# Kernel tuning notes

Hardware: AMD Instinct MI355X
Metric: run time of the kernel (lower is better)

The kernel has to match this reference:

```python
import jax, jax.numpy as jnp
import numpy as np

N = 50000
DIN, DH, DOUT = 128, 128, 64
DEPTH = 3
TEMP = 1.0
WEIGHT = 0.5
LN_EPS = 1e-5
E_RAND = 1_600_000


def setup_inputs() -> dict:
    key = jax.random.key(0)
    ks = jax.random.split(key, 16)
    x = jax.random.normal(ks[0], (N, DIN), jnp.float32)
    # random edges + ring (guarantees degree >= 2 after symmetrization)
    src = jax.random.randint(ks[1], (E_RAND,), 0, N)
    dst = jax.random.randint(ks[2], (E_RAND,), 0, N)
    ring = jnp.arange(N)
    s = jnp.concatenate([src, ring])
    d = jnp.concatenate([dst, (ring + 1) % N])
    edge_index = jnp.stack([jnp.concatenate([s, d]), jnp.concatenate([d, s])]).astype(jnp.int64)  # [2, 3.3M], symmetric

    def glorot(k, i, o):
        return jax.random.normal(k, (i, o), jnp.float32) * jnp.sqrt(2.0 / (i + o)).astype(jnp.float32)

    return {
        "x": x, "edge_index": edge_index,
        "W0": glorot(ks[3], DIN, DH), "b0": jnp.zeros((DH,), jnp.float32),
        "W1": glorot(ks[4], DH, DH),  "b1": jnp.zeros((DH,), jnp.float32),
        "W2": glorot(ks[5], DH, DH),  "b2": jnp.zeros((DH,), jnp.float32),
        "W_out": glorot(ks[6], DH, DOUT), "b_out": jnp.zeros((DOUT,), jnp.float32),
        "gamma": jnp.ones((DH,), jnp.float32), "beta": jnp.zeros((DH,), jnp.float32),
    }


def _seg(vals, idx):
    return jax.ops.segment_sum(vals, idx, num_segments=N)


def _gcn_conv(h_in, W, b, src, dst):
    # PyG GCNConv: self-loops, sym norm D^-1/2 (A+I) D^-1/2
    h = h_in @ W
    ones = jnp.ones(src.shape, jnp.float32)
    deg = _seg(ones, dst) + 1.0  # degree incl. self-loop
    dinv = jax.lax.rsqrt(deg)
    msg = h[src] * (dinv[src] * dinv[dst])[:, None]
    return _seg(msg, dst) + h * (1.0 / deg)[:, None] + b


def _layernorm(x, g, b):
    m = jnp.mean(x, axis=-1, keepdims=True)
    v = jnp.mean((x - m) ** 2, axis=-1, keepdims=True)
    return (x - m) * jax.lax.rsqrt(v + LN_EPS) * g + b


def reference(x, edge_index, W0, b0, W1, b1, W2, b2, W_out, b_out, gamma, beta):
    src, dst = edge_index[0], edge_index[1]
    h = x
    for W, b in ((W0, b0), (W1, b1), (W2, b2)):
        h = _layernorm(jax.nn.relu(_gcn_conv(h, W, b, src, dst)), gamma, beta)
    emb = _gcn_conv(h, W_out, b_out, src, dst)  # [N, DOUT]

    # --- entropy gradient (edge-list form of the dense-A einsums) ---
    ones = jnp.ones(src.shape, jnp.float32)
    deg_adj = _seg(ones, src)                     # row sums of A (no self-loops)
    en_norm = 1.0 / jnp.sqrt(deg_adj * DH)        # uses hidden_dim, as in the original

    rn2 = jnp.sum(emb * emb, axis=1)              # ||X_i||^2
    dot = jnp.sum(emb[src] * emb[dst], axis=1)    # <X_i, X_j> per edge
    res1 = deg_adj * rn2
    res2 = _seg(dot, src)
    res3 = _seg(rn2[dst], src)
    energies = 0.5 * (res1 - 2.0 * res2 + res3) * en_norm  # normalize_energies=True

    logits = -energies / TEMP
    P = jax.nn.softmax(logits, axis=0) + 1e-10
    logP = jnp.log(P)
    S = -jnp.sum(P * logP)
    Pbar = P * (S + logP)                         # [N]

    nsumX = _seg(emb[dst], src)                   # sum_j A_ij X_j
    nsumP = _seg(Pbar[dst], src)                  # sum_j A_ij Pbar_j
    XP = emb * Pbar[:, None]
    g1 = deg_adj[:, None] * XP
    g2 = emb * nsumP[:, None]
    g3 = Pbar[:, None] * nsumX
    g4 = _seg(XP[dst], src)
    grad_S = (g1 + g2 - g3 - g4) / TEMP * en_norm[:, None]

    return emb + WEIGHT * grad_S
```

## Files before the change

kernel.cpp:

```cpp
#include <hip/hip_runtime.h>
#include <hip/hip_fp16.h>

#define DIN 128
#define DH  128
#define DFO 64
#define LN_EPS 1e-5f
#define WEIGHT 0.5f

#define MAXB  104
#define CAPB  48
#define FLUSH 32
#define SENT  0xFFFFFFFFu

typedef unsigned int uint32;
typedef unsigned short ushort16;

__device__ __forceinline__ float h_lo(uint32 u) { return __half2float(__ushort_as_half((unsigned short)(u & 0xFFFFu))); }
__device__ __forceinline__ float h_hi(uint32 u) { return __half2float(__ushort_as_half((unsigned short)(u >> 16))); }
__device__ __forceinline__ uint32 pack_h2(float a, float b) {
  return (uint32)__half_as_ushort(__float2half_rn(a)) | ((uint32)__half_as_ushort(__float2half_rn(b)) << 16);
}
__device__ __forceinline__ int sb(uint32 u, int k) { return ((int)(u << (24 - 8 * k))) >> 24; }

__device__ __forceinline__ float wave_sum(float v) {
  #pragma unroll
  for (int off = 32; off > 0; off >>= 1) v += __shfl_xor(v, off);
  return v;
}
__device__ __forceinline__ float wave_max(float v) {
  #pragma unroll
  for (int off = 32; off > 0; off >>= 1) v = fmaxf(v, __shfl_xor(v, off));
  return v;
}

__device__ __forceinline__ void fq16(float* a, uint4 u, float w) {
  #pragma unroll
  for (int k = 0; k < 4; ++k) a[k]      = fmaf((float)sb(u.x, k), w, a[k]);
  #pragma unroll
  for (int k = 0; k < 4; ++k) a[4 + k]  = fmaf((float)sb(u.y, k), w, a[4 + k]);
  #pragma unroll
  for (int k = 0; k < 4; ++k) a[8 + k]  = fmaf((float)sb(u.z, k), w, a[8 + k]);
  #pragma unroll
  for (int k = 0; k < 4; ++k) a[12 + k] = fmaf((float)sb(u.w, k), w, a[12 + k]);
}

__global__ __launch_bounds__(64) void k_prep(const float* __restrict__ g, const float* __restrict__ b,
                      const float* __restrict__ W1, const float* __restrict__ W2,
                      const float* __restrict__ Wo, float* __restrict__ Wg1,
                      float* __restrict__ Wg2, float* __restrict__ Wgo,
                      float* __restrict__ vecs) {
  int c = blockIdx.x * 64 + threadIdx.x;
  const float* W; float* Wg; float* gv; float* bv; int ld; int col;
  if (c < 128)      { W = W1; Wg = Wg1; gv = vecs;       bv = vecs + 128; ld = 128; col = c; }
  else if (c < 256) { W = W2; Wg = Wg2; gv = vecs + 256; bv = vecs + 384; ld = 128; col = c - 128; }
  else              { W = Wo; Wg = Wgo; gv = vecs + 512; bv = vecs + 576; ld = 64;  col = c - 256; }
  float gs = 0.f, bs = 0.f;
  for (int k = 0; k < 128; ++k) {
    float w = W[k * ld + col];
    float gk = g[k];
    Wg[k * ld + col] = gk * w;
    gs += gk * w;
    bs += b[k] * w;
  }
  gv[col] = gs; bv[col] = bs;
}

__global__ __launch_bounds__(256) void k_bin3(const int* __restrict__ src, const int* __restrict__ dst,
                       int E2, int nbc, int GCAP, int* __restrict__ gbcnt,
                       uint32* __restrict__ gpairs) {
  __shared__ uint32 lbuf[MAXB][CAPB];
  __shared__ int lcnt[MAXB];
  __shared__ int fbase[MAXB];
  __shared__ int fm[MAXB];
  __shared__ short flist[MAXB];
  __shared__ int fn;
  int wv = threadIdx.x >> 6, ln = threadIdx.x & 63;
  for (int b = threadIdx.x; b < nbc; b += 256) lcnt[b] = 0;
  __syncthreads();

  for (int base = blockIdx.x * 256; base < E2; base += gridDim.x * 256) {
    int i = base + threadIdx.x;
    if (i < E2) {
      int s = src[i], d = dst[i];
      int b0 = s >> 9;
      uint32 v0 = ((uint32)(s & 511) << 16) | (uint32)d;
      int sl = atomicAdd(&lcnt[b0], 1);
      if (sl < CAPB) lbuf[b0][sl] = v0;
      else { int g = atomicAdd(&gbcnt[b0 * 16], 1); gpairs[(size_t)b0 * GCAP + g] = v0; }
      int b1 = d >> 9;
      uint32 v1 = ((uint32)(d & 511) << 16) | (uint32)s;
      sl = atomicAdd(&lcnt[b1], 1);
      if (sl < CAPB) lbuf[b1][sl] = v1;
      else { int g = atomicAdd(&gbcnt[b1 * 16], 1); gpairs[(size_t)b1 * GCAP + g] = v1; }
    }
    if (threadIdx.x == 0) fn = 0;
    __syncthreads();
    if (threadIdx.x < nbc) {
      int m = lcnt[threadIdx.x];
      if (m >= FLUSH) {
        if (m > CAPB) m = CAPB;
        int r = (m + 15) & ~15;
        fbase[threadIdx.x] = atomicAdd(&gbcnt[threadIdx.x * 16], r);
        fm[threadIdx.x] = m;
        int fi = atomicAdd(&fn, 1);
        flist[fi] = (short)threadIdx.x;
      }
    }
    __syncthreads();
    int nf = fn;
    for (int fi = wv; fi < nf; fi += 4) {
      int b = flist[fi];
      int m = fm[b], r = (m + 15) & ~15, g = fbase[b];
      if (ln < r)
        gpairs[(size_t)b * GCAP + g + ln] = (ln < m) ? lbuf[b][ln] : SENT;
    }
    __syncthreads();
    if (threadIdx.x < nbc && lcnt[threadIdx.x] >= FLUSH) lcnt[threadIdx.x] = 0;
    __syncthreads();
  }
  if (threadIdx.x < nbc) {
    int m = lcnt[threadIdx.x]; if (m > CAPB) m = CAPB;
    fm[threadIdx.x] = m;
    if (m > 0) {
      int r = (m + 15) & ~15;
      fbase[threadIdx.x] = atomicAdd(&gbcnt[threadIdx.x * 16], r);
    }
  }
  __syncthreads();
  for (int b = wv; b < nbc; b += 4) {
    int m = fm[b];
    if (m > 0) {
      int r = (m + 15) & ~15, g = fbase[b];
      if (ln < r)
        gpairs[(size_t)b * GCAP + g + ln] = (ln < m) ? lbuf[b][ln] : SENT;
    }
  }
}

__global__ __launch_bounds__(1024) void k_csr(const uint32* __restrict__ gpairs, const int* __restrict__ gbcnt,
                      int GCAP, int GCAPC, int N, int* __restrict__ rowbeg, int* __restrict__ rowcnt,
                      float* __restrict__ dinv, float* __restrict__ cntf, ushort16* __restrict__ col) {
  __shared__ int hist[512];
  __shared__ int pos[512];
  int b = blockIdx.x, tid = threadIdx.x;
  if (tid < 512) hist[tid] = 0;
  __syncthreads();
  int m = gbcnt[b * 16];
  const uint32* pp = gpairs + (size_t)b * GCAP;
  for (int t = tid; t < m; t += 1024) {
    uint32 v = pp[t];
    if (v != SENT) atomicAdd(&hist[v >> 16], 1);
  }
  __syncthreads();
  int cnt = (tid < 512) ? hist[tid] : 0;
  for (int off = 1; off < 512; off <<= 1) {
    int u = (tid >= off && tid < 512) ? hist[tid - off] : 0;
    __syncthreads();
    if (tid < 512) hist[tid] += u;
    __syncthreads();
  }
  int cbase = b * GCAPC;
  if (tid < 512) {
    int excl = hist[tid] - cnt;
    pos[tid] = excl;
    int node = (b << 9) + tid;
    if (node < N) {
      rowbeg[node] = cbase + excl;
      rowcnt[node] = cnt;
      cntf[node] = (float)cnt;
      dinv[node] = rsqrtf((float)cnt + 1.0f);
    }
  }
  __syncthreads();
  for (int t = tid; t < m; t += 1024) {
    uint32 v = pp[t];
    if (v != SENT) {
      int sl = atomicAdd(&pos[v >> 16], 1);
      col[cbase + sl] = (ushort16)(v & 0xFFFFu);
    }
  }
}

template <int COLS, int MODE>
__global__ __launch_bounds__(256) void k_gemm(const void* __restrict__ Ap, const float* __restrict__ W,
                            const float* __restrict__ dinv, const float2* __restrict__ stats,
                            const float* __restrict__ gW, const float* __restrict__ bW,
                            uint32* __restrict__ qout, float* __restrict__ qsc, int N) {
  const int CG  = COLS / 4;
  const int RG  = 256 / CG;
  const int RPT = 64 / RG;
  __shared__ float4 At4[64 * 32];
  int t = threadIdx.x;
  int rbase = blockIdx.x * 64;
  #pragma unroll
  for (int i2 = 0; i2 < 8; ++i2) {
    int idx = t + 256 * i2;
    int row = idx >> 5, c4i = idx & 31;
    int gr = rbase + row;
    float4 v = make_float4(0.f, 0.f, 0.f, 0.f);
    if (gr < N) {
      if (MODE == 1) {
        const uint2* A2 = (const uint2*)Ap;
        uint2 p = A2[(size_t)(c4i >> 4) * N * 16 + (size_t)gr * 16 + (c4i & 15)];
        v = make_float4(h_lo(p.x), h_hi(p.x), h_lo(p.y), h_hi(p.y));
      } else {
        v = ((const float4*)Ap)[(size_t)gr * 32 + c4i];
      }
    }
    At4[idx] = v;
  }
  __syncthreads();
  int c4 = t % CG, rg = t / CG;
  float acc[RPT][4];
  #pragma unroll
  for (int r = 0; r < RPT; ++r) { acc[r][0] = acc[r][1] = acc[r][2] = acc[r][3] = 0.f; }
  const float4* W4 = (const float4*)W;
  #pragma unroll 2
  for (int k4 = 0; k4 < 32; ++k4) {
    float4 w0 = W4[(k4 * 4 + 0) * CG + c4];
    float4 w1 = W4[(k4 * 4 + 1) * CG + c4];
    float4 w2 = W4[(k4 * 4 + 2) * CG + c4];
    float4 w3 = W4[(k4 * 4 + 3) * CG + c4];
    #pragma unroll
    for (int r = 0; r < RPT; ++r) {
      float4 av = At4[(rg * RPT + r) * 32 + k4];
      acc[r][0] = fmaf(av.x, w0.x, acc[r][0]); acc[r][0] = fmaf(av.y, w1.x, acc[r][0]);
      acc[r][0] = fmaf(av.z, w2.x, acc[r][0]); acc[r][0] = fmaf(av.w, w3.x, acc[r][0]);
      acc[r][1] = fmaf(av.x, w0.y, acc[r][1]); acc[r][1] = fmaf(av.y, w1.y, acc[r][1]);
      acc[r][1] = fmaf(av.z, w2.y, acc[r][1]); acc[r][1] = fmaf(av.w, w3.y, acc[r][1]);
      acc[r][2] = fmaf(av.x, w0.z, acc[r][2]); acc[r][2] = fmaf(av.y, w1.z, acc[r][2]);
      acc[r][2] = fmaf(av.z, w2.z, acc[r][2]); acc[r][2] = fmaf(av.w, w3.z, acc[r][2]);
      acc[r][3] = fmaf(av.x, w0.w, acc[r][3]); acc[r][3] = fmaf(av.y, w1.w, acc[r][3]);
      acc[r][3] = fmaf(av.z, w2.w, acc[r][3]); acc[r][3] = fmaf(av.w, w3.w, acc[r][3]);
    }
  }
  float4 g4 = make_float4(0.f, 0.f, 0.f, 0.f), b4 = make_float4(0.f, 0.f, 0.f, 0.f);
  if (MODE == 1) { g4 = ((const float4*)gW)[c4]; b4 = ((const float4*)bW)[c4]; }
  int pl = c4 >> 4, slot = c4 & 15;
  #pragma unroll
  for (int r = 0; r < RPT; ++r) {
    int gr = rbase + rg * RPT + r;
    float o0 = 0.f, o1 = 0.f, o2 = 0.f, o3 = 0.f;
    if (gr < N) {
      float s = dinv[gr];
      if (MODE == 1) {
        float2 st = stats[gr];
        o0 = s * (st.y * (acc[r][0] - st.x * g4.x) + b4.x);
        o1 = s * (st.y * (acc[r][1] - st.x * g4.y) + b4.y);
        o2 = s * (st.y * (acc[r][2] - st.x * g4.z) + b4.z);
        o3 = s * (st.y * (acc[r][3] - st.x * g4.w) + b4.w);
      } else {
        o0 = acc[r][0] * s; o1 = acc[r][1] * s; o2 = acc[r][2] * s; o3 = acc[r][3] * s;
      }
    }
    float mx = fmaxf(fmaxf(fabsf(o0), fabsf(o1)), fmaxf(fabsf(o2), fabsf(o3)));
    #pragma unroll
    for (int m = 1; m < CG; m <<= 1) mx = fmaxf(mx, __shfl_xor(mx, m));
    if (gr < N) {
      float inv = (mx > 0.f) ? 127.f / mx : 0.f;
      int q0 = (int)rintf(o0 * inv), q1 = (int)rintf(o1 * inv);
      int q2 = (int)rintf(o2 * inv), q3 = (int)rintf(o3 * inv);
      uint32 qw = (uint32)(q0 & 255) | ((uint32)(q1 & 255) << 8) |
                  ((uint32)(q2 & 255) << 16) | ((uint32)(q3 & 255) << 24);
      qout[(size_t)pl * N * 16 + (size_t)gr * 16 + slot] = qw;
      if (c4 == 0) qsc[gr] = mx * (1.f / 127.f);
    }
  }
}

template <int PLANE>
__global__ __launch_bounds__(64) void k_aggh(const uint4* __restrict__ hq4, const float* __restrict__ hsc,
                      const int* __restrict__ rowbeg, const int* __restrict__ rowcnt,
                      const ushort16* __restrict__ col, const float* __restrict__ dinv,
                      const float* __restrict__ bias, uint4* __restrict__ vh4,
                      float2* __restrict__ ss, float2* __restrict__ stats, int N) {
  int i = blockIdx.x, lane = threadIdx.x;
  int f4 = lane & 3, sl = lane >> 2;
  const uint4* hp = hq4 + (size_t)PLANE * N * 4;
  int beg = rowbeg[i], end = beg + rowcnt[i];
  float a[16];
  #pragma unroll
  for (int k = 0; k < 16; ++k) a[k] = 0.f;
  if (lane < 4) fq16(a, hp[(size_t)i * 4 + f4], hsc[i]);
  int t = beg + sl;
  for (; t + 16 < end; t += 32) {
    int j0 = col[t], j1 = col[t + 16];
    float s0 = hsc[j0], s1 = hsc[j1];
    uint4 u0 = hp[(size_t)j0 * 4 + f4];
    uint4 u1 = hp[(size_t)j1 * 4 + f4];
    fq16(a, u0, s0); fq16(a, u1, s1);
  }
  if (t < end) { int j = col[t]; fq16(a, hp[(size_t)j * 4 + f4], hsc[j]); }
  #pragma unroll
  for (int k = 0; k < 16; ++k) {
    a[k] += __shfl_xor(a[k], 4);  a[k] += __shfl_xor(a[k], 8);
    a[k] += __shfl_xor(a[k], 16); a[k] += __shfl_xor(a[k], 32);
  }
  if (lane < 4) {
    float di = dinv[i];
    const float4* bb = (const float4*)bias + PLANE * 16 + f4 * 4;
    float s = 0.f, s2 = 0.f;
    #pragma unroll
    for (int q = 0; q < 4; ++q) {
      float4 b4 = bb[q];
      float v0 = fmaxf(fmaf(a[q*4+0], di, b4.x), 0.f);
      float v1 = fmaxf(fmaf(a[q*4+1], di, b4.y), 0.f);
      float v2 = fmaxf(fmaf(a[q*4+2], di, b4.z), 0.f);
      float v3 = fmaxf(fmaf(a[q*4+3], di, b4.w), 0.f);
      a[q*4+0] = v0; a[q*4+1] = v1; a[q*4+2] = v2; a[q*4+3] = v3;
      s += (v0 + v1) + (v2 + v3);
      s2 += (v0*v0 + v1*v1) + (v2*v2 + v3*v3);
    }
    s += __shfl_xor(s, 1); s2 += __shfl_xor(s2, 1);
    s += __shfl_xor(s, 2); s2 += __shfl_xor(s2, 2);
    uint4 o0, o1;
    o0.x = pack_h2(a[0], a[1]);  o0.y = pack_h2(a[2], a[3]);
    o0.z = pack_h2(a[4], a[5]);  o0.w = pack_h2(a[6], a[7]);
    o1.x = pack_h2(a[8], a[9]);  o1.y = pack_h2(a[10], a[11]);
    o1.z = pack_h2(a[12], a[13]); o1.w = pack_h2(a[14], a[15]);
    vh4[(size_t)PLANE * N * 8 + (size_t)i * 8 + f4 * 2]     = o0;
    vh4[(size_t)PLANE * N * 8 + (size_t)i * 8 + f4 * 2 + 1] = o1;
    if (lane == 0) {
      if (PLANE == 0) {
        ss[i] = make_float2(s, s2);
      } else {
        float2 qq = ss[i];
        float S = s + qq.x, S2 = s2 + qq.y;
        float mean = S * (1.f / 128.f);
        float var  = S2 * (1.f / 128.f) - mean * mean;
        stats[i] = make_float2(mean, rsqrtf(var + LN_EPS));
      }
    }
  }
}

__global__ __launch_bounds__(64) void k_agg_out(const uint4* __restrict__ hq4, const float* __restrict__ hsc,
                          const int* __restrict__ rowbeg, const int* __restrict__ rowcnt,
                          const ushort16* __restrict__ col, const float* __restrict__ dinv,
                          const float* __restrict__ bias, float* __restrict__ embf,
                          uint4* __restrict__ embq4, float* __restrict__ esc,
                          float* __restrict__ rn2, int N) {
  int i = blockIdx.x, lane = threadIdx.x;
  int f4 = lane & 3, sl = lane >> 2;
  int beg = rowbeg[i], end = beg + rowcnt[i];
  float a[16];
  #pragma unroll
  for (int k = 0; k < 16; ++k) a[k] = 0.f;
  if (lane < 4) fq16(a, hq4[(size_t)i * 4 + f4], hsc[i]);
  int t = beg + sl;
  for (; t + 16 < end; t += 32) {
    int j0 = col[t], j1 = col[t + 16];
    float s0 = hsc[j0], s1 = hsc[j1];
    uint4 u0 = hq4[(size_t)j0 * 4 + f4];
    uint4 u1 = hq4[(size_t)j1 * 4 + f4];
    fq16(a, u0, s0); fq16(a, u1, s1);
  }
  if (t < end) { int j = col[t]; fq16(a, hq4[(size_t)j * 4 + f4], hsc[j]); }
  #pragma unroll
  for (int k = 0; k < 16; ++k) {
    a[k] += __shfl_xor(a[k], 4);  a[k] += __shfl_xor(a[k], 8);
    a[k] += __shfl_xor(a[k], 16); a[k] += __shfl_xor(a[k], 32);
  }
  if (lane < 4) {
    float di = dinv[i];
    const float4* bb = (const float4*)bias + f4 * 4;
    float s2 = 0.f, mx = 0.f;
    #pragma unroll
    for (int q = 0; q < 4; ++q) {
      float4 b4 = bb[q];
      float e0 = fmaf(a[q*4+0], di, b4.x);
      float e1 = fmaf(a[q*4+1], di, b4.y);
      float e2 = fmaf(a[q*4+2], di, b4.z);
      float e3 = fmaf(a[q*4+3], di, b4.w);
      a[q*4+0] = e0; a[q*4+1] = e1; a[q*4+2] = e2; a[q*4+3] = e3;
      s2 += (e0*e0 + e1*e1) + (e2*e2 + e3*e3);
      mx = fmaxf(mx, fmaxf(fmaxf(fabsf(e0), fabsf(e1)), fmaxf(fabsf(e2), fabsf(e3))));
      ((float4*)embf)[(size_t)i * 16 + f4 * 4 + q] = make_float4(e0, e1, e2, e3);
    }
    s2 += __shfl_xor(s2, 1); s2 += __shfl_xor(s2, 2);
    mx = fmaxf(mx, __shfl_xor(mx, 1)); mx = fmaxf(mx, __shfl_xor(mx, 2));
    float inv = (mx > 0.f) ? 127.f / mx : 0.f;
    uint4 qo;
    uint32* qw = (uint32*)&qo;
    #pragma unroll
    for (int q = 0; q < 4; ++q) {
      int q0 = (int)rintf(a[q*4+0] * inv), q1 = (int)rintf(a[q*4+1] * inv);
      int q2 = (int)rintf(a[q*4+2] * inv), q3 = (int)rintf(a[q*4+3] * inv);
      qw[q] = (uint32)(q0 & 255) | ((uint32)(q1 & 255) << 8) |
              ((uint32)(q2 & 255) << 16) | ((uint32)(q3 & 255) << 24);
    }
    embq4[(size_t)i * 4 + f4] = qo;
    if (lane == 0) { rn2[i] = s2; esc[i] = mx * (1.f / 127.f); }
  }
}

__global__ __launch_bounds__(64) void k_passA(const float* __restrict__ embf, const uint4* __restrict__ embq4,
                        const float* __restrict__ esc, const int* __restrict__ rowbeg,
                        const int* __restrict__ rowcnt, const ushort16* __restrict__ col,
                        const float* __restrict__ rn2, const float* __restrict__ cntf,
                        float* __restrict__ nsumX, float* __restrict__ logits, int N) {
  int i = blockIdx.x, lane = threadIdx.x;
  int f4 = lane & 3, sl = lane >> 2;
  int beg = rowbeg[i], end = beg + rowcnt[i];
  float a[16];
  #pragma unroll
  for (int k = 0; k < 16; ++k) a[k] = 0.f;
  float r3 = 0.f;
  int t = beg + sl;
  for (; t + 16 < end; t += 32) {
    int j0 = col[t], j1 = col[t + 16];
    float s0 = esc[j0], s1 = esc[j1];
    uint4 u0 = embq4[(size_t)j0 * 4 + f4];
    uint4 u1 = embq4[(size_t)j1 * 4 + f4];
    fq16(a, u0, s0); fq16(a, u1, s1);
    if (f4 == 0) r3 += rn2[j0] + rn2[j1];
  }
  if (t < end) {
    int j = col[t];
    fq16(a, embq4[(size_t)j * 4 + f4], esc[j]);
    if (f4 == 0) r3 += rn2[j];
  }
  #pragma unroll
  for (int k = 0; k < 16; ++k) {
    a[k] += __shfl_xor(a[k], 4);  a[k] += __shfl_xor(a[k], 8);
    a[k] += __shfl_xor(a[k], 16); a[k] += __shfl_xor(a[k], 32);
  }
  r3 = wave_sum(r3);
  if (lane < 4) {
    float dd = 0.f;
    #pragma unroll
    for (int q = 0; q < 4; ++q) {
      float4 e = ((const float4*)embf)[(size_t)i * 16 + f4 * 4 + q];
      dd += e.x * a[q*4+0] + e.y * a[q*4+1] + e.z * a[q*4+2] + e.w * a[q*4+3];
      ((float4*)nsumX)[(size_t)i * 16 + f4 * 4 + q] = make_float4(a[q*4+0], a[q*4+1], a[q*4+2], a[q*4+3]);
    }
    dd += __shfl_xor(dd, 1); dd += __shfl_xor(dd, 2);
    if (lane == 0) {
      float c = cntf[i];
      float en = rsqrtf(c * 128.0f);
      logits[i] = -0.5f * (c * rn2[i] - 2.f * dd + r3) * en;
    }
  }
}

__global__ __launch_bounds__(256) void k_sm1(const float* __restrict__ logits, int N,
                                             float4* __restrict__ partials) {
  int idx = blockIdx.x * 256 + threadIdx.x;
  int w = threadIdx.x >> 6, ln = threadIdx.x & 63;
  float x = (idx < N) ? logits[idx] : -3.4e38f;
  float m = wave_max(x);
  __shared__ float red[3][4];
  if (ln == 0) red[0][w] = m;
  __syncthreads();
  float M = fmaxf(fmaxf(red[0][0], red[0][1]), fmaxf(red[0][2], red[0][3]));
  float ev = (idx < N) ? expf(x - M) : 0.f;
  float tv = (idx < N) ? (x - M) * ev : 0.f;
  float se = wave_sum(ev), st = wave_sum(tv);
  if (ln == 0) { red[1][w] = se; red[2][w] = st; }
  __syncthreads();
  if (threadIdx.x == 0)
    partials[blockIdx.x] = make_float4(M, red[1][0] + red[1][1] + red[1][2] + red[1][3],
                                          red[2][0] + red[2][1] + red[2][2] + red[2][3], 0.f);
}

__global__ __launch_bounds__(256) void k_sm2(const float4* __restrict__ partials, int nb,
                                             float* __restrict__ scal) {
  int tid = threadIdx.x;
  int w = tid >> 6, ln = tid & 63;
  float4 p = (tid < nb) ? partials[tid] : make_float4(-3.4e38f, 0.f, 0.f, 0.f);
  float m = wave_max(p.x);
  __shared__ float red[3][4];
  if (ln == 0) red[0][w] = m;
  __syncthreads();
  float M = fmaxf(fmaxf(red[0][0], red[0][1]), fmaxf(red[0][2], red[0][3]));
  float sc = (tid < nb) ? expf(p.x - M) : 0.f;
  float se = p.y * sc;
  float tt = (p.z + (p.x - M) * p.y) * sc;
  se = wave_sum(se); tt = wave_sum(tt);
  if (ln == 0) { red[1][w] = se; red[2][w] = tt; }
  __syncthreads();
  if (tid == 0) {
    float SE = red[1][0] + red[1][1] + red[1][2] + red[1][3];
    float TT = red[2][0] + red[2][1] + red[2][2] + red[2][3];
    scal[0] = M;
    scal[1] = SE;
    scal[2] = logf(SE) - TT / SE;
  }
}

__global__ __launch_bounds__(256) void k_pbar(const float* __restrict__ logits, int N,
                     const float* __restrict__ scal, float* __restrict__ Pb) {
  float M = scal[0], SE = scal[1], S = scal[2];
  int i = blockIdx.x * blockDim.x + threadIdx.x;
  int stride = gridDim.x * blockDim.x;
  for (; i < N; i += stride) {
    float p = expf(logits[i] - M) / SE + 1e-10f;
    Pb[i] = p * (S + logf(p));
  }
}

__global__ __launch_bounds__(64) void k_passB(const float* __restrict__ embf, const uint4* __restrict__ embq4,
                        const float* __restrict__ esc, const int* __restrict__ rowbeg,
                        const int* __restrict__ rowcnt, const ushort16* __restrict__ col,
                        const float* __restrict__ Pb, const float* __restrict__ cntf,
                        float* __restrict__ outp, int N) {
  int i = blockIdx.x, lane = threadIdx.x;
  int f4 = lane & 3, sl = lane >> 2;
  int beg = rowbeg[i], end = beg + rowcnt[i];
  float a[16];
  #pragma unroll
  for (int k = 0; k < 16; ++k) a[k] = 0.f;
  float sp = 0.f;
  int t = beg + sl;
  for (; t + 16 < end; t += 32) {
    int j0 = col[t], j1 = col[t + 16];
    float p0 = Pb[j0], p1 = Pb[j1];
    float w0 = p0 * esc[j0], w1 = p1 * esc[j1];
    uint4 u0 = embq4[(size_t)j0 * 4 + f4];
    uint4 u1 = embq4[(size_t)j1 * 4 + f4];
    fq16(a, u0, w0); fq16(a, u1, w1);
    if (f4 == 0) sp += p0 + p1;
  }
  if (t < end) {
    int j = col[t];
    float p = Pb[j];
    fq16(a, embq4[(size_t)j * 4 + f4], p * esc[j]);
    if (f4 == 0) sp += p;
  }
  #pragma unroll
  for (int k = 0; k < 16; ++k) {
    a[k] += __shfl_xor(a[k], 4);  a[k] += __shfl_xor(a[k], 8);
    a[k] += __shfl_xor(a[k], 16); a[k] += __shfl_xor(a[k], 32);
  }
  sp = wave_sum(sp);
  if (lane < 4) {
    float Pi = Pb[i];
    float c = cntf[i];
    float wgt = WEIGHT * rsqrtf(c * 128.0f);
    #pragma unroll
    for (int q = 0; q < 4; ++q) {
      float4 e = ((const float4*)embf)[(size_t)i * 16 + f4 * 4 + q];
      float4 n = ((const float4*)outp)[(size_t)i * 16 + f4 * 4 + q];
      float g0 = c * e.x * Pi + e.x * sp - Pi * n.x - a[q*4+0];
      float g1 = c * e.y * Pi + e.y * sp - Pi * n.y - a[q*4+1];
      float g2 = c * e.z * Pi + e.z * sp - Pi * n.z - a[q*4+2];
      float g3 = c * e.w * Pi + e.w * sp - Pi * n.w - a[q*4+3];
      ((float4*)outp)[(size_t)i * 16 + f4 * 4 + q] =
          make_float4(fmaf(wgt, g0, e.x), fmaf(wgt, g1, e.y), fmaf(wgt, g2, e.z), fmaf(wgt, g3, e.w));
    }
  }
}

extern "C" void kernel_launch(void* const* d_in, const int* in_sizes, int n_in,
                              void* d_out, int out_size, void* d_ws, size_t ws_size,
                              hipStream_t stream) {
  const float* x     = (const float*)d_in[0];
  const int*   ei    = (const int*)d_in[1];
  const float* W0    = (const float*)d_in[2];
  const float* b0    = (const float*)d_in[3];
  const float* W1    = (const float*)d_in[4];
  const float* b1    = (const float*)d_in[5];
  const float* W2    = (const float*)d_in[6];
  const float* b2    = (const float*)d_in[7];
  const float* Wo    = (const float*)d_in[8];
  const float* bo    = (const float*)d_in[9];
  const float* gamma = (const float*)d_in[10];
  const float* beta  = (const float*)d_in[11];

  int N = in_sizes[0] / DIN;
  int E = in_sizes[1] / 2;
  int E2 = E / 2;
  const int* src = ei;
  const int* dst = ei + E;
  int nbc = (N + 511) >> 9;
  int perb = E / nbc;
  int GCAP  = ((perb + perb / 3 + 8192) + 15) & ~15;
  int GCAPC = perb + 4096;

  char* w = (char*)d_ws;
  auto alloc = [&](size_t bytes) { void* p = w; w += (bytes + 255) & ~(size_t)255; return p; };
  char* regA = (char*)alloc((size_t)N * 128 * 2);
  char* regB = (char*)alloc((size_t)N * 64 * 2);
  char* pad  = (char*)alloc((size_t)2 * 1024 * 1024);
  (void)pad;
  ushort16* colx = (ushort16*)alloc((size_t)nbc * GCAPC * 2);
  int*    rowbeg = (int*)alloc((size_t)N * 4);
  int*    rowcnt = (int*)alloc((size_t)N * 4);
  float*  dinv   = (float*)alloc((size_t)N * 4);
  float*  cntf   = (float*)alloc((size_t)N * 4);
  float*  rn2    = (float*)alloc((size_t)N * 4);
  float*  logits = (float*)alloc((size_t)N * 4);
  float*  Pb     = (float*)alloc((size_t)N * 4);
  float*  hsc    = (float*)alloc((size_t)N * 4);
  float*  oscq   = (float*)alloc((size_t)N * 4);
  float*  esc    = (float*)alloc((size_t)N * 4);
  float2* ss     = (float2*)alloc((size_t)N * 8);
  float2* stats  = (float2*)alloc((size_t)N * 8);
  float*  Wg1    = (float*)alloc(128 * 128 * 4);
  float*  Wg2    = (float*)alloc(128 * 128 * 4);
  float*  Wgo    = (float*)alloc(128 * 64 * 4);
  float*  vecs   = (float*)alloc(640 * 4);
  int*    gbcnt  = (int*)alloc((size_t)MAXB * 16 * 4);
  float4* partials = (float4*)alloc(4096);
  float*  scal   = (float*)alloc(256);

  uint32* gpairs = (uint32*)regA;
  uint4*  vh4    = (uint4*)regA;
  float*  embf   = (float*)regA;
  uint32* hq     = (uint32*)regB;
  uint32* hoq    = (uint32*)regB;
  uint4*  embq4  = (uint4*)(regB + (size_t)N * 64);

  hipMemsetAsync(gbcnt, 0, (size_t)MAXB * 64, stream);
  k_prep<<<5, 64, 0, stream>>>(gamma, beta, W1, W2, Wo, Wg1, Wg2, Wgo, vecs);
  k_bin3<<<1024, 256, 0, stream>>>(src, dst, E2, nbc, GCAP, gbcnt, gpairs);
  k_csr<<<nbc, 1024, 0, stream>>>(gpairs, gbcnt, GCAP, GCAPC, N, rowbeg, rowcnt, dinv, cntf, colx);

  int gblk = (N + 63) / 64;

  k_gemm<DH, 0><<<gblk, 256, 0, stream>>>(x, W0, dinv, nullptr, nullptr, nullptr, hq, hsc, N);
  k_aggh<0><<<N, 64, 0, stream>>>((const uint4*)hq, hsc, rowbeg, rowcnt, colx, dinv, b0, vh4, ss, stats, N);
  k_aggh<1><<<N, 64, 0, stream>>>((const uint4*)hq, hsc, rowbeg, rowcnt, colx, dinv, b0, vh4, ss, stats, N);
  k_gemm<DH, 1><<<gblk, 256, 0, stream>>>(vh4, Wg1, dinv, stats, vecs, vecs + 128, hq, hsc, N);
  k_aggh<0><<<N, 64, 0, stream>>>((const uint4*)hq, hsc, rowbeg, rowcnt, colx, dinv, b1, vh4, ss, stats, N);
  k_aggh<1><<<N, 64, 0, stream>>>((const uint4*)hq, hsc, rowbeg, rowcnt, colx, dinv, b1, vh4, ss, stats, N);
  k_gemm<DH, 1><<<gblk, 256, 0, stream>>>(vh4, Wg2, dinv, stats, vecs + 256, vecs + 384, hq, hsc, N);
  k_aggh<0><<<N, 64, 0, stream>>>((const uint4*)hq, hsc, rowbeg, rowcnt, colx, dinv, b2, vh4, ss, stats, N);
  k_aggh<1><<<N, 64, 0, stream>>>((const uint4*)hq, hsc, rowbeg, rowcnt, colx, dinv, b2, vh4, ss, stats, N);
  k_gemm<DFO, 1><<<gblk, 256, 0, stream>>>(vh4, Wgo, dinv, stats, vecs + 512, vecs + 576, hoq, oscq, N);
  k_agg_out<<<N, 64, 0, stream>>>((const uint4*)hoq, oscq, rowbeg, rowcnt, colx, dinv, bo, embf, embq4, esc, rn2, N);

  k_passA<<<N, 64, 0, stream>>>(embf, embq4, esc, rowbeg, rowcnt, colx, rn2, cntf, (float*)d_out, logits, N);
  int nb = (N + 255) / 256;
  k_sm1<<<nb, 256, 0, stream>>>(logits, N, partials);
  k_sm2<<<1, 256, 0, stream>>>(partials, nb, scal);
  k_pbar<<<256, 256, 0, stream>>>(logits, N, scal, Pb);
  k_passB<<<N, 64, 0, stream>>>(embf, embq4, esc, rowbeg, rowcnt, colx, Pb, cntf, (float*)d_out, N);
}
```

Baseline: 669.4 us.

## Merge split-plane hidden aggregation into one full-row pass; pack per-node scalars

The hidden-layer gather previously ran in two feature-plane halves (two kernel launches per layer, each gathering 64 features per neighbour), with LayerNorm stats combined across launches. The change switches the quantized hidden and fp16 activation buffers to a row-contiguous layout and does one aggregation per layer with 8 lanes covering the full 128-feature row. The aim is to halve the per-layer gather of column indices and scales and drop three launches. It also packs the emb scale with ||x||^2, and Pbar with Pbar*scale, into float2 arrays so each neighbour needs one scalar load instead of two. The trade-off is a larger per-layer gather footprint that may fit worse in cache than the half-width planes did.

Result: faster. 565.4 us (-15.5%).

```diff
diff --git a/kernel.cpp b/kernel.cpp
--- a/kernel.cpp
+++ b/kernel.cpp
@@ -200,8 +200,7 @@
     float4 v = make_float4(0.f, 0.f, 0.f, 0.f);
     if (gr < N) {
       if (MODE == 1) {
-        const uint2* A2 = (const uint2*)Ap;
-        uint2 p = A2[(size_t)(c4i >> 4) * N * 16 + (size_t)gr * 16 + (c4i & 15)];
+        uint2 p = ((const uint2*)Ap)[(size_t)gr * 32 + c4i];
         v = make_float4(h_lo(p.x), h_hi(p.x), h_lo(p.y), h_hi(p.y));
       } else {
         v = ((const float4*)Ap)[(size_t)gr * 32 + c4i];
@@ -236,7 +235,6 @@
   }
   float4 g4 = make_float4(0.f, 0.f, 0.f, 0.f), b4 = make_float4(0.f, 0.f, 0.f, 0.f);
   if (MODE == 1) { g4 = ((const float4*)gW)[c4]; b4 = ((const float4*)bW)[c4]; }
-  int pl = c4 >> 4, slot = c4 & 15;
   #pragma unroll
   for (int r = 0; r < RPT; ++r) {
     int gr = rbase + rg * RPT + r;
@@ -262,43 +260,42 @@
       int q2 = (int)rintf(o2 * inv), q3 = (int)rintf(o3 * inv);
       uint32 qw = (uint32)(q0 & 255) | ((uint32)(q1 & 255) << 8) |
                   ((uint32)(q2 & 255) << 16) | ((uint32)(q3 & 255) << 24);
-      qout[(size_t)pl * N * 16 + (size_t)gr * 16 + slot] = qw;
+      qout[(size_t)gr * CG + c4] = qw;
       if (c4 == 0) qsc[gr] = mx * (1.f / 127.f);
     }
   }
 }
 
-template <int PLANE>
 __global__ __launch_bounds__(64) void k_aggh(const uint4* __restrict__ hq4, const float* __restrict__ hsc,
                       const int* __restrict__ rowbeg, const int* __restrict__ rowcnt,
                       const ushort16* __restrict__ col, const float* __restrict__ dinv,
                       const float* __restrict__ bias, uint4* __restrict__ vh4,
-                      float2* __restrict__ ss, float2* __restrict__ stats, int N) {
+                      float2* __restrict__ stats, int N) {
   int i = blockIdx.x, lane = threadIdx.x;
-  int f4 = lane & 3, sl = lane >> 2;
-  const uint4* hp = hq4 + (size_t)PLANE * N * 4;
+  int f = lane & 7, sl = lane >> 3;
   int beg = rowbeg[i], end = beg + rowcnt[i];
   float a[16];
   #pragma unroll
   for (int k = 0; k < 16; ++k) a[k] = 0.f;
-  if (lane < 4) fq16(a, hp[(size_t)i * 4 + f4], hsc[i]);
+  if (lane < 8) fq16(a, hq4[(size_t)i * 8 + f], hsc[i]);
   int t = beg + sl;
-  for (; t + 16 < end; t += 32) {
-    int j0 = col[t], j1 = col[t + 16];
+  for (; t + 8 < end; t += 16) {
+    int j0 = col[t], j1 = col[t + 8];
     float s0 = hsc[j0], s1 = hsc[j1];
-    uint4 u0 = hp[(size_t)j0 * 4 + f4];
-    uint4 u1 = hp[(size_t)j1 * 4 + f4];
+    uint4 u0 = hq4[(size_t)j0 * 8 + f];
+    uint4 u1 = hq4[(size_t)j1 * 8 + f];
     fq16(a, u0, s0); fq16(a, u1, s1);
   }
-  if (t < end) { int j = col[t]; fq16(a, hp[(size_t)j * 4 + f4], hsc[j]); }
+  if (t < end) { int j = col[t]; fq16(a, hq4[(size_t)j * 8 + f], hsc[j]); }
   #pragma unroll
   for (int k = 0; k < 16; ++k) {
-    a[k] += __shfl_xor(a[k], 4);  a[k] += __shfl_xor(a[k], 8);
-    a[k] += __shfl_xor(a[k], 16); a[k] += __shfl_xor(a[k], 32);
-  }
-  if (lane < 4) {
+    a[k] += __shfl_xor(a[k], 8);
+    a[k] += __shfl_xor(a[k], 16);
+    a[k] += __shfl_xor(a[k], 32);
+  }
+  if (lane < 8) {
     float di = dinv[i];
-    const float4* bb = (const float4*)bias + PLANE * 16 + f4 * 4;
+    const float4* bb = (const float4*)bias + f * 4;
     float s = 0.f, s2 = 0.f;
     #pragma unroll
     for (int q = 0; q < 4; ++q) {
@@ -313,23 +310,18 @@
     }
     s += __shfl_xor(s, 1); s2 += __shfl_xor(s2, 1);
     s += __shfl_xor(s, 2); s2 += __shfl_xor(s2, 2);
+    s += __shfl_xor(s, 4); s2 += __shfl_xor(s2, 4);
     uint4 o0, o1;
-    o0.x = pack_h2(a[0], a[1]);  o0.y = pack_h2(a[2], a[3]);
-    o0.z = pack_h2(a[4], a[5]);  o0.w = pack_h2(a[6], a[7]);
-    o1.x = pack_h2(a[8], a[9]);  o1.y = pack_h2(a[10], a[11]);
+    o0.x = pack_h2(a[0], a[1]);   o0.y = pack_h2(a[2], a[3]);
+    o0.z = pack_h2(a[4], a[5]);   o0.w = pack_h2(a[6], a[7]);
+    o1.x = pack_h2(a[8], a[9]);   o1.y = pack_h2(a[10], a[11]);
     o1.z = pack_h2(a[12], a[13]); o1.w = pack_h2(a[14], a[15]);
-    vh4[(size_t)PLANE * N * 8 + (size_t)i * 8 + f4 * 2]     = o0;
-    vh4[(size_t)PLANE * N * 8 + (size_t)i * 8 + f4 * 2 + 1] = o1;
+    vh4[(size_t)i * 16 + f * 2]     = o0;
+    vh4[(size_t)i * 16 + f * 2 + 1] = o1;
     if (lane == 0) {
-      if (PLANE == 0) {
-        ss[i] = make_float2(s, s2);
-      } else {
-        float2 qq = ss[i];
-        float S = s + qq.x, S2 = s2 + qq.y;
-        float mean = S * (1.f / 128.f);
-        float var  = S2 * (1.f / 128.f) - mean * mean;
-        stats[i] = make_float2(mean, rsqrtf(var + LN_EPS));
-      }
+      float mean = s * (1.f / 128.f);
+      float var  = s2 * (1.f / 128.f) - mean * mean;
+      stats[i] = make_float2(mean, rsqrtf(var + LN_EPS));
     }
   }
 }
@@ -338,8 +330,7 @@
                           const int* __restrict__ rowbeg, const int* __restrict__ rowcnt,
                           const ushort16* __restrict__ col, const float* __restrict__ dinv,
                           const float* __restrict__ bias, float* __restrict__ embf,
-                          uint4* __restrict__ embq4, float* __restrict__ esc,
-                          float* __restrict__ rn2, int N) {
+                          uint4* __restrict__ embq4, float2* __restrict__ escr2, int N) {
   int i = blockIdx.x, lane = threadIdx.x;
   int f4 = lane & 3, sl = lane >> 2;
   int beg = rowbeg[i], end = beg + rowcnt[i];
@@ -390,15 +381,15 @@
               ((uint32)(q2 & 255) << 16) | ((uint32)(q3 & 255) << 24);
     }
     embq4[(size_t)i * 4 + f4] = qo;
-    if (lane == 0) { rn2[i] = s2; esc[i] = mx * (1.f / 127.f); }
+    if (lane == 0) escr2[i] = make_float2(mx * (1.f / 127.f), s2);
   }
 }
 
 __global__ __launch_bounds__(64) void k_passA(const float* __restrict__ embf, const uint4* __restrict__ embq4,
-                        const float* __restrict__ esc, const int* __restrict__ rowbeg,
+                        const float2* __restrict__ escr2, const int* __restrict__ rowbeg,
                         const int* __restrict__ rowcnt, const ushort16* __restrict__ col,
-                        const float* __restrict__ rn2, const float* __restrict__ cntf,
-                        float* __restrict__ nsumX, float* __restrict__ logits, int N) {
+                        const float* __restrict__ cntf, float* __restrict__ nsumX,
+                        float* __restrict__ logits, int N) {
   int i = blockIdx.x, lane = threadIdx.x;
   int f4 = lane & 3, sl = lane >> 2;
   int beg = rowbeg[i], end = beg + rowcnt[i];
@@ -409,16 +400,17 @@
   int t = beg + sl;
   for (; t + 16 < end; t += 32) {
     int j0 = col[t], j1 = col[t + 16];
-    float s0 = esc[j0], s1 = esc[j1];
+    float2 er0 = escr2[j0], er1 = escr2[j1];
     uint4 u0 = embq4[(size_t)j0 * 4 + f4];
     uint4 u1 = embq4[(size_t)j1 * 4 + f4];
-    fq16(a, u0, s0); fq16(a, u1, s1);
-    if (f4 == 0) r3 += rn2[j0] + rn2[j1];
+    fq16(a, u0, er0.x); fq16(a, u1, er1.x);
+    if (f4 == 0) r3 += er0.y + er1.y;
   }
   if (t < end) {
     int j = col[t];
-    fq16(a, embq4[(size_t)j * 4 + f4], esc[j]);
-    if (f4 == 0) r3 += rn2[j];
+    float2 er = escr2[j];
+    fq16(a, embq4[(size_t)j * 4 + f4], er.x);
+    if (f4 == 0) r3 += er.y;
   }
   #pragma unroll
   for (int k = 0; k < 16; ++k) {
@@ -438,7 +430,7 @@
     if (lane == 0) {
       float c = cntf[i];
       float en = rsqrtf(c * 128.0f);
-      logits[i] = -0.5f * (c * rn2[i] - 2.f * dd + r3) * en;
+      logits[i] = -0.5f * (c * escr2[i].y - 2.f * dd + r3) * en;
     }
   }
 }
@@ -489,21 +481,22 @@
 }
 
 __global__ __launch_bounds__(256) void k_pbar(const float* __restrict__ logits, int N,
-                     const float* __restrict__ scal, float* __restrict__ Pb) {
+                     const float* __restrict__ scal, const float2* __restrict__ escr2,
+                     float2* __restrict__ pw2) {
   float M = scal[0], SE = scal[1], S = scal[2];
   int i = blockIdx.x * blockDim.x + threadIdx.x;
   int stride = gridDim.x * blockDim.x;
   for (; i < N; i += stride) {
     float p = expf(logits[i] - M) / SE + 1e-10f;
-    Pb[i] = p * (S + logf(p));
+    float pb = p * (S + logf(p));
+    pw2[i] = make_float2(pb, pb * escr2[i].x);
   }
 }
 
 __global__ __launch_bounds__(64) void k_passB(const float* __restrict__ embf, const uint4* __restrict__ embq4,
-                        const float* __restrict__ esc, const int* __restrict__ rowbeg,
+                        const float2* __restrict__ pw2, const int* __restrict__ rowbeg,
                         const int* __restrict__ rowcnt, const ushort16* __restrict__ col,
-                        const float* __restrict__ Pb, const float* __restrict__ cntf,
-                        float* __restrict__ outp, int N) {
+                        const float* __restrict__ cntf, float* __restrict__ outp, int N) {
   int i = blockIdx.x, lane = threadIdx.x;
   int f4 = lane & 3, sl = lane >> 2;
   int beg = rowbeg[i], end = beg + rowcnt[i];
@@ -514,18 +507,17 @@
   int t = beg + sl;
   for (; t + 16 < end; t += 32) {
     int j0 = col[t], j1 = col[t + 16];
-    float p0 = Pb[j0], p1 = Pb[j1];
-    float w0 = p0 * esc[j0], w1 = p1 * esc[j1];
+    float2 p0 = pw2[j0], p1 = pw2[j1];
     uint4 u0 = embq4[(size_t)j0 * 4 + f4];
     uint4 u1 = embq4[(size_t)j1 * 4 + f4];
-    fq16(a, u0, w0); fq16(a, u1, w1);
-    if (f4 == 0) sp += p0 + p1;
+    fq16(a, u0, p0.y); fq16(a, u1, p1.y);
+    if (f4 == 0) sp += p0.x + p1.x;
   }
   if (t < end) {
     int j = col[t];
-    float p = Pb[j];
-    fq16(a, embq4[(size_t)j * 4 + f4], p * esc[j]);
-    if (f4 == 0) sp += p;
+    float2 p = pw2[j];
+    fq16(a, embq4[(size_t)j * 4 + f4], p.y);
+    if (f4 == 0) sp += p.x;
   }
   #pragma unroll
   for (int k = 0; k < 16; ++k) {
@@ -534,7 +526,7 @@
   }
   sp = wave_sum(sp);
   if (lane < 4) {
-    float Pi = Pb[i];
+    float Pi = pw2[i].x;
     float c = cntf[i];
     float wgt = WEIGHT * rsqrtf(c * 128.0f);
     #pragma unroll
@@ -580,21 +572,19 @@
   char* w = (char*)d_ws;
   auto alloc = [&](size_t bytes) { void* p = w; w += (bytes + 255) & ~(size_t)255; return p; };
   char* regA = (char*)alloc((size_t)N * 128 * 2);
-  char* regB = (char*)alloc((size_t)N * 64 * 2);
-  char* pad  = (char*)alloc((size_t)2 * 1024 * 1024);
+  char* regB = (char*)alloc((size_t)N * 128);
+  char* pad  = (char*)alloc((size_t)3 * 1024 * 1024);
   (void)pad;
   ushort16* colx = (ushort16*)alloc((size_t)nbc * GCAPC * 2);
   int*    rowbeg = (int*)alloc((size_t)N * 4);
   int*    rowcnt = (int*)alloc((size_t)N * 4);
   float*  dinv   = (float*)alloc((size_t)N * 4);
   float*  cntf   = (float*)alloc((size_t)N * 4);
-  float*  rn2    = (float*)alloc((size_t)N * 4);
   float*  logits = (float*)alloc((size_t)N * 4);
-  float*  Pb     = (float*)alloc((size_t)N * 4);
   float*  hsc    = (float*)alloc((size_t)N * 4);
   float*  oscq   = (float*)alloc((size_t)N * 4);
-  float*  esc    = (float*)alloc((size_t)N * 4);
-  float2* ss     = (float2*)alloc((size_t)N * 8);
+  float2* escr2  = (float2*)alloc((size_t)N * 8);
+  float2* pw2    = (float2*)alloc((size_t)N * 8);
   float2* stats  = (float2*)alloc((size_t)N * 8);
   float*  Wg1    = (float*)alloc(128 * 128 * 4);
   float*  Wg2    = (float*)alloc(128 * 128 * 4);
@@ -619,21 +609,18 @@
   int gblk = (N + 63) / 64;
 
   k_gemm<DH, 0><<<gblk, 256, 0, stream>>>(x, W0, dinv, nullptr, nullptr, nullptr, hq, hsc, N);
-  k_aggh<0><<<N, 64, 0, stream>>>((const uint4*)hq, hsc, rowbeg, rowcnt, colx, dinv, b0, vh4, ss, stats, N);
-  k_aggh<1><<<N, 64, 0, stream>>>((const uint4*)hq, hsc, rowbeg, rowcnt, colx, dinv, b0, vh4, ss, stats, N);
+  k_aggh<<<N, 64, 0, stream>>>((const uint4*)hq, hsc, rowbeg, rowcnt, colx, dinv, b0, vh4, stats, N);
   k_gemm<DH, 1><<<gblk, 256, 0, stream>>>(vh4, Wg1, dinv, stats, vecs, vecs + 128, hq, hsc, N);
-  k_aggh<0><<<N, 64, 0, stream>>>((const uint4*)hq, hsc, rowbeg, rowcnt, colx, dinv, b1, vh4, ss, stats, N);
-  k_aggh<1><<<N, 64, 0, stream>>>((const uint4*)hq, hsc, rowbeg, rowcnt, colx, dinv, b1, vh4, ss, stats, N);
+  k_aggh<<<N, 64, 0, stream>>>((const uint4*)hq, hsc, rowbeg, rowcnt, colx, dinv, b1, vh4, stats, N);
   k_gemm<DH, 1><<<gblk, 256, 0, stream>>>(vh4, Wg2, dinv, stats, vecs + 256, vecs + 384, hq, hsc, N);
-  k_aggh<0><<<N, 64, 0, stream>>>((const uint4*)hq, hsc, rowbeg, rowcnt, colx, dinv, b2, vh4, ss, stats, N);
-  k_aggh<1><<<N, 64, 0, stream>>>((const uint4*)hq, hsc, rowbeg, rowcnt, colx, dinv, b2, vh4, ss, stats, N);
+  k_aggh<<<N, 64, 0, stream>>>((const uint4*)hq, hsc, rowbeg, rowcnt, colx, dinv, b2, vh4, stats, N);
   k_gemm<DFO, 1><<<gblk, 256, 0, stream>>>(vh4, Wgo, dinv, stats, vecs + 512, vecs + 576, hoq, oscq, N);
-  k_agg_out<<<N, 64, 0, stream>>>((const uint4*)hoq, oscq, rowbeg, rowcnt, colx, dinv, bo, embf, embq4, esc, rn2, N);
-
-  k_passA<<<N, 64, 0, stream>>>(embf, embq4, esc, rowbeg, rowcnt, colx, rn2, cntf, (float*)d_out, logits, N);
+  k_agg_out<<<N, 64, 0, stream>>>((const uint4*)hoq, oscq, rowbeg, rowcnt, colx, dinv, bo, embf, embq4, escr2, N);
+
+  k_passA<<<N, 64, 0, stream>>>(embf, embq4, escr2, rowbeg, rowcnt, colx, cntf, (float*)d_out, logits, N);
   int nb = (N + 255) / 256;
   k_sm1<<<nb, 256, 0, stream>>>(logits, N, partials);
   k_sm2<<<1, 256, 0, stream>>>(partials, nb, scal);
-  k_pbar<<<256, 256, 0, stream>>>(logits, N, scal, Pb);
-  k_passB<<<N, 64, 0, stream>>>(embf, embq4, esc, rowbeg, rowcnt, colx, Pb, cntf, (float*)d_out, N);
-}
+  k_pbar<<<256, 256, 0, stream>>>(logits, N, scal, escr2, pw2);
+  k_passB<<<N, 64, 0, stream>>>(embf, embq4, pw2, rowbeg, rowcnt, colx, cntf, (float*)d_out, N);
+}
```
